# Kernel optimization log

Measured on AMD Instinct MI355X. Metric: run time of the kernel, lower is better.

## Reference

```python
import jax, jax.numpy as jnp
import numpy as np

H, C = 5, 12            # heads, head_size
N_NODES, N_EDGES = 100000, 1600000
F_NODE, F_EDGE = 128, 32
HID, N_CLASSES = 16, 2


def _lin_init(key, din, dout, bias=True):
    k1, k2 = jax.random.split(key)
    s = 1.0 / np.sqrt(din)
    W = jax.random.uniform(k1, (din, dout), minval=-s, maxval=s, dtype=jnp.float32)
    if bias:
        b = jax.random.uniform(k2, (dout,), minval=-s, maxval=s, dtype=jnp.float32)
        return W, b
    return W


def setup_inputs() -> dict:
    key = jax.random.key(0)
    ks = jax.random.split(key, 8)
    d = {}
    d["x"] = jax.random.normal(ks[0], (N_NODES, F_NODE), dtype=jnp.float32)
    d["edge_index"] = jax.random.randint(ks[1], (2, N_EDGES), 0, N_NODES)
    d["edge_attr"] = jax.random.normal(ks[2], (N_EDGES, F_EDGE), dtype=jnp.float32)
    HC = H * C
    for i, din in [(1, F_NODE), (2, HC)]:
        kk = jax.random.split(ks[2 + i], 5)
        d[f"Wq{i}"], d[f"bq{i}"] = _lin_init(kk[0], din, HC)
        d[f"Wk{i}"], d[f"bk{i}"] = _lin_init(kk[1], din, HC)
        d[f"Wv{i}"], d[f"bv{i}"] = _lin_init(kk[2], din, HC)
        d[f"We{i}"] = _lin_init(kk[3], F_EDGE, HC, bias=False)  # lin_edge has no bias in PyG
        d[f"Ws{i}"], d[f"bs{i}"] = _lin_init(kk[4], din, HC)    # root/skip linear
    d["W1"], d["b1"] = _lin_init(ks[6], HC, HID)
    d["W2"], d["b2"] = _lin_init(ks[7], HID, N_CLASSES)
    return d


def _transformer_conv(x, src, dst, edge_attr, Wq, bq, Wk, bk, Wv, bv, We, Ws, bs):
    # PyG TransformerConv, concat=True, root_weight=True, beta=False, dropout=0
    N = x.shape[0]
    q = (x @ Wq + bq).reshape(N, H, C)
    k = (x @ Wk + bk).reshape(N, H, C)
    v = (x @ Wv + bv).reshape(N, H, C)
    e = (edge_attr @ We).reshape(-1, H, C)          # [E,H,C]
    kj = k[src] + e                                  # per-edge key
    vj = v[src] + e                                  # per-edge value
    alpha = jnp.einsum('ehc,ehc->eh', q[dst], kj) / jnp.sqrt(jnp.asarray(C, x.dtype))
    # segment-softmax over incoming edges of each destination node
    amax = jax.ops.segment_max(alpha, dst, num_segments=N)          # [N,H]
    w = jnp.exp(alpha - amax[dst])
    denom = jax.ops.segment_sum(w, dst, num_segments=N)             # [N,H]
    w = w / (denom[dst] + 1e-16)
    out = jax.ops.segment_sum(vj * w[:, :, None], dst, num_segments=N).reshape(N, H * C)
    return out + x @ Ws + bs                                         # skip/root connection


def reference(x, edge_index, edge_attr,
              Wq1, bq1, Wk1, bk1, Wv1, bv1, We1, Ws1, bs1,
              Wq2, bq2, Wk2, bk2, Wv2, bv2, We2, Ws2, bs2,
              W1, b1, W2, b2):
    src, dst = edge_index[0], edge_index[1]
    h = jax.nn.relu(_transformer_conv(x, src, dst, edge_attr, Wq1, bq1, Wk1, bk1, Wv1, bv1, We1, Ws1, bs1))
    h = jax.nn.relu(_transformer_conv(h, src, dst, edge_attr, Wq2, bq2, Wk2, bk2, Wv2, bv2, We2, Ws2, bs2))
    h = jax.nn.relu(h @ W1 + b1)
    return h @ W2 + b2
```

## Files before the change

kernel.cpp:

```cpp
#include <hip/hip_runtime.h>
#include <hip/hip_bf16.h>
#include <cstddef>

#define NN 100000
#define NE 1600000
#define NH 5
#define NC 12
#define HC 60
#define FN 128
#define FE 32
#define HID 16
#define NCLS 2

template<int DIN>
__global__ __launch_bounds__(256) void qkvs_kernel(
    const float* __restrict__ X,
    const float* __restrict__ Wq, const float* __restrict__ bq,
    const float* __restrict__ Wk, const float* __restrict__ bk,
    const float* __restrict__ Wv, const float* __restrict__ bv,
    const float* __restrict__ Ws, const float* __restrict__ bs,
    float* __restrict__ q, float* __restrict__ k,
    float* __restrict__ v, float* __restrict__ s)
{
    constexpr int NB = 8;
    __shared__ float xs[NB][DIN];
    const int n0 = blockIdx.x * NB;
    for (int i = threadIdx.x; i < NB * DIN; i += 256) {
        const int m = i / DIN, r = i - m * DIN;
        const int node = n0 + m;
        xs[m][r] = (node < NN) ? X[(size_t)node * DIN + r] : 0.f;
    }
    __syncthreads();

    const int j = threadIdx.x;
    if (j >= 240) return;
    const int mat = j / 60, col = j - mat * 60;
    const float* W; const float* b; float* out;
    switch (mat) {
        case 0:  W = Wq; b = bq; out = q; break;
        case 1:  W = Wk; b = bk; out = k; break;
        case 2:  W = Wv; b = bv; out = v; break;
        default: W = Ws; b = bs; out = s; break;
    }
    float acc[NB];
    #pragma unroll
    for (int m = 0; m < NB; ++m) acc[m] = 0.f;
    #pragma unroll 4
    for (int r = 0; r < DIN; ++r) {
        const float w = W[r * 60 + col];
        #pragma unroll
        for (int m = 0; m < NB; ++m) acc[m] = fmaf(xs[m][r], w, acc[m]);
    }
    const float bb = b[col];
    #pragma unroll
    for (int m = 0; m < NB; ++m) {
        const int node = n0 + m;
        if (node < NN) out[(size_t)node * 60 + col] = acc[m] + bb;
    }
}

__global__ __launch_bounds__(256) void hist_kernel(
    const int* __restrict__ ei, int* __restrict__ cnt)
{
    const int e = blockIdx.x * 256 + threadIdx.x;
    if (e < NE) atomicAdd(&cnt[ei[NE + e]], 1);
}

__global__ __launch_bounds__(1024) void scan1_kernel(
    const int* __restrict__ cnt, int* __restrict__ excl, int* __restrict__ bsum)
{
    __shared__ int sh[1024];
    const int i = blockIdx.x * 1024 + threadIdx.x;
    const int v = (i < NN) ? cnt[i] : 0;
    sh[threadIdx.x] = v;
    __syncthreads();
    for (int off = 1; off < 1024; off <<= 1) {
        const int t = (threadIdx.x >= off) ? sh[threadIdx.x - off] : 0;
        __syncthreads();
        sh[threadIdx.x] += t;
        __syncthreads();
    }
    if (i < NN) excl[i] = sh[threadIdx.x] - v;
    if (threadIdx.x == 1023) bsum[blockIdx.x] = sh[1023];
}

__global__ void scan2_kernel(int* __restrict__ bsum, int nb, int* __restrict__ start)
{
    if (threadIdx.x == 0 && blockIdx.x == 0) {
        int acc = 0;
        for (int b = 0; b < nb; ++b) { const int t = bsum[b]; bsum[b] = acc; acc += t; }
        start[NN] = acc;
    }
}

__global__ __launch_bounds__(1024) void scan3_kernel(
    int* __restrict__ start, const int* __restrict__ bsum)
{
    const int i = blockIdx.x * 1024 + threadIdx.x;
    if (i < NN) start[i] += bsum[blockIdx.x];
}

__global__ __launch_bounds__(256) void scatter_kernel(
    const int* __restrict__ ei, int* __restrict__ cursor,
    int* __restrict__ perm, int* __restrict__ srcs)
{
    const int e = blockIdx.x * 256 + threadIdx.x;
    if (e >= NE) return;
    const int d = ei[NE + e];
    const int pos = atomicAdd(&cursor[d], 1);
    perm[pos] = e;
    srcs[pos] = ei[e];
}

__global__ __launch_bounds__(256) void agg_kernel(
    const int* __restrict__ perm, const int* __restrict__ srcs,
    const int* __restrict__ start,
    const float* __restrict__ ea, const float* __restrict__ We,
    const float* __restrict__ q, const float* __restrict__ k,
    const float* __restrict__ v, const float* __restrict__ sk,
    float* __restrict__ hout)
{
    const int wv    = threadIdx.x >> 6;
    const int lane  = threadIdx.x & 63;
    const int n     = blockIdx.x * 4 + wv;
    const int hc    = (lane < 60) ? lane : 0;
    const int hd    = hc / NC;
    const int hbase = hd * NC;
    const int c     = hc - hbase;

    const int r1 = hbase + ((c + 6) % 12);
    const int r2 = hbase + ((c + 3) % 12);
    const int r3 = hbase + ((c + 1) % 3);
    const int r4 = hbase + ((c + 2) % 3);

    float Wcol[FE];
    #pragma unroll
    for (int r = 0; r < FE; ++r) Wcol[r] = We[r * 60 + hc];

    const float qv = q[(size_t)n * 60 + hc];
    const float sv = sk[(size_t)n * 60 + hc];

    const int s0 = __builtin_amdgcn_readfirstlane(start[n]);
    const int s1 = __builtin_amdgcn_readfirstlane(start[n + 1]);

    float acc = 0.f, den = 0.f;

    for (int c0 = s0; c0 < s1; c0 += 64) {
        const int cnt = min(64, s1 - c0);

        int myE = 0, myS = 0;
        if (c0 + lane < s1) { myE = perm[c0 + lane]; myS = srcs[c0 + lane]; }

        float eaA[FE], eaB[FE], kvA, vvA, kvB, vvB;

        {
            const int e = __builtin_amdgcn_readfirstlane(__shfl(myE, 0));
            const int s = __builtin_amdgcn_readfirstlane(__shfl(myS, 0));
            const float* __restrict__ er = ea + (size_t)e * FE;
            #pragma unroll
            for (int r = 0; r < FE; ++r) eaA[r] = er[r];
            kvA = k[(size_t)s * 60 + hc];
            vvA = v[(size_t)s * 60 + hc];
        }

        for (int t = 0; t < cnt; t += 2) {
            if (t + 1 < cnt) {
                const int e = __builtin_amdgcn_readfirstlane(__shfl(myE, t + 1));
                const int s = __builtin_amdgcn_readfirstlane(__shfl(myS, t + 1));
                const float* __restrict__ er = ea + (size_t)e * FE;
                #pragma unroll
                for (int r = 0; r < FE; ++r) eaB[r] = er[r];
                kvB = k[(size_t)s * 60 + hc];
                vvB = v[(size_t)s * 60 + hc];
            }
            {
                float e0 = 0.f, e1 = 0.f;
                #pragma unroll
                for (int r = 0; r < FE; r += 2) {
                    e0 = fmaf(eaA[r],     Wcol[r],     e0);
                    e1 = fmaf(eaA[r + 1], Wcol[r + 1], e1);
                }
                const float eacc = e0 + e1;
                const float p  = qv * (kvA + eacc);
                const float f1 = p  + __shfl(p,  r1);
                const float f2 = f1 + __shfl(f1, r2);
                const float a  = f2 + __shfl(f2, r3) + __shfl(f2, r4);
                const float w  = __expf(fmaf(a, 0.28867513459481287f, -20.0f));
                acc = fmaf(w, vvA + eacc, acc);
                den += w;
            }
            if (t + 2 < cnt) {
                const int e = __builtin_amdgcn_readfirstlane(__shfl(myE, t + 2));
                const int s = __builtin_amdgcn_readfirstlane(__shfl(myS, t + 2));
                const float* __restrict__ er = ea + (size_t)e * FE;
                #pragma unroll
                for (int r = 0; r < FE; ++r) eaA[r] = er[r];
                kvA = k[(size_t)s * 60 + hc];
                vvA = v[(size_t)s * 60 + hc];
            }
            if (t + 1 < cnt) {
                float e0 = 0.f, e1 = 0.f;
                #pragma unroll
                for (int r = 0; r < FE; r += 2) {
                    e0 = fmaf(eaB[r],     Wcol[r],     e0);
                    e1 = fmaf(eaB[r + 1], Wcol[r + 1], e1);
                }
                const float eacc = e0 + e1;
                const float p  = qv * (kvB + eacc);
                const float f1 = p  + __shfl(p,  r1);
                const float f2 = f1 + __shfl(f1, r2);
                const float a  = f2 + __shfl(f2, r3) + __shfl(f2, r4);
                const float w  = __expf(fmaf(a, 0.28867513459481287f, -20.0f));
                acc = fmaf(w, vvB + eacc, acc);
                den += w;
            }
        }
    }

    if (lane < 60)
        hout[(size_t)n * 60 + hc] = fmaxf(acc / (den + 1e-16f) + sv, 0.f);
}

__global__ __launch_bounds__(256) void mlp_kernel(
    const float* __restrict__ h,
    const float* __restrict__ W1, const float* __restrict__ b1,
    const float* __restrict__ W2, const float* __restrict__ b2,
    float* __restrict__ out)
{
    __shared__ float sW1[60 * HID];
    __shared__ float sb1[HID];
    __shared__ float sW2[HID * NCLS];
    __shared__ float sb2[NCLS];
    for (int i = threadIdx.x; i < 60 * HID; i += 256) sW1[i] = W1[i];
    if (threadIdx.x < HID)        sb1[threadIdx.x] = b1[threadIdx.x];
    if (threadIdx.x < HID * NCLS) sW2[threadIdx.x] = W2[threadIdx.x];
    if (threadIdx.x < NCLS)       sb2[threadIdx.x] = b2[threadIdx.x];
    __syncthreads();

    const int n = blockIdx.x * 256 + threadIdx.x;
    if (n >= NN) return;
    const float* __restrict__ hr = h + (size_t)n * 60;
    float hv[60];
    #pragma unroll
    for (int i = 0; i < 15; ++i) {
        const float4 t = ((const float4*)hr)[i];
        hv[4 * i + 0] = t.x; hv[4 * i + 1] = t.y;
        hv[4 * i + 2] = t.z; hv[4 * i + 3] = t.w;
    }
    float o0 = sb2[0], o1 = sb2[1];
    for (int j = 0; j < HID; ++j) {
        float t = sb1[j];
        #pragma unroll
        for (int i = 0; i < 60; ++i) t = fmaf(hv[i], sW1[i * HID + j], t);
        t = fmaxf(t, 0.f);
        o0 = fmaf(t, sW2[2 * j + 0], o0);
        o1 = fmaf(t, sW2[2 * j + 1], o1);
    }
    out[(size_t)n * 2 + 0] = o0;
    out[(size_t)n * 2 + 1] = o1;
}

extern "C" void kernel_launch(void* const* d_in, const int* in_sizes, int n_in,
                              void* d_out, int out_size, void* d_ws, size_t ws_size,
                              hipStream_t stream)
{
    const float* x   = (const float*)d_in[0];
    const int*   ei  = (const int*)  d_in[1];
    const float* ea  = (const float*)d_in[2];
    const float* Wq1 = (const float*)d_in[3];  const float* bq1 = (const float*)d_in[4];
    const float* Wk1 = (const float*)d_in[5];  const float* bk1 = (const float*)d_in[6];
    const float* Wv1 = (const float*)d_in[7];  const float* bv1 = (const float*)d_in[8];
    const float* We1 = (const float*)d_in[9];
    const float* Ws1 = (const float*)d_in[10]; const float* bs1 = (const float*)d_in[11];
    const float* Wq2 = (const float*)d_in[12]; const float* bq2 = (const float*)d_in[13];
    const float* Wk2 = (const float*)d_in[14]; const float* bk2 = (const float*)d_in[15];
    const float* Wv2 = (const float*)d_in[16]; const float* bv2 = (const float*)d_in[17];
    const float* We2 = (const float*)d_in[18];
    const float* Ws2 = (const float*)d_in[19]; const float* bs2 = (const float*)d_in[20];
    const float* W1  = (const float*)d_in[21]; const float* b1  = (const float*)d_in[22];
    const float* W2  = (const float*)d_in[23]; const float* b2  = (const float*)d_in[24];
    float* out = (float*)d_out;

    float* ws = (float*)d_ws;
    const size_t NHC = (size_t)NN * 60;
    float* qb = ws;
    float* kb = qb + NHC;
    float* vb = kb + NHC;
    float* sb = vb + NHC;
    float* h0 = sb + NHC;
    int* cnt    = (int*)(h0 + NHC);
    int* startp = cnt + NN;
    int* cursor = startp + NN + 1;
    int* bsum   = cursor + NN;
    int* perm   = bsum + 128;
    int* srcs   = perm + NE;

    const int qkvs_blocks = (NN + 7) / 8;
    const int e256_blocks = NE / 256;
    const int scan_blocks = (NN + 1023) / 1024;
    const int agg_blocks  = NN / 4;
    const int mlp_blocks  = (NN + 255) / 256;

    hipMemsetAsync(cnt, 0, (size_t)NN * sizeof(int), stream);
    hist_kernel<<<e256_blocks, 256, 0, stream>>>(ei, cnt);
    scan1_kernel<<<scan_blocks, 1024, 0, stream>>>(cnt, startp, bsum);
    scan2_kernel<<<1, 64, 0, stream>>>(bsum, scan_blocks, startp);
    scan3_kernel<<<scan_blocks, 1024, 0, stream>>>(startp, bsum);
    hipMemcpyAsync(cursor, startp, (size_t)NN * sizeof(int),
                   hipMemcpyDeviceToDevice, stream);
    scatter_kernel<<<e256_blocks, 256, 0, stream>>>(ei, cursor, perm, srcs);

    qkvs_kernel<FN><<<qkvs_blocks, 256, 0, stream>>>(
        x, Wq1, bq1, Wk1, bk1, Wv1, bv1, Ws1, bs1, qb, kb, vb, sb);
    agg_kernel<<<agg_blocks, 256, 0, stream>>>(
        perm, srcs, startp, ea, We1, qb, kb, vb, sb, h0);

    qkvs_kernel<HC><<<qkvs_blocks, 256, 0, stream>>>(
        h0, Wq2, bq2, Wk2, bk2, Wv2, bv2, Ws2, bs2, qb, kb, vb, sb);
    agg_kernel<<<agg_blocks, 256, 0, stream>>>(
        perm, srcs, startp, ea, We2, qb, kb, vb, sb, h0);

    mlp_kernel<<<mlp_blocks, 256, 0, stream>>>(h0, W1, b1, W2, b2, out);
}
```

Baseline: 1.398 ms.

## Pre-permute edge attributes into CSR order and deepen k/v prefetch in aggregation

Adds a kernel that gathers edge_attr rows into destination-sorted order once, so both aggregation passes read edge features contiguously instead of through the perm indirection. The aggregation loop now prefetches source k/v two edges ahead and uses readlane in place of shfl+readfirstlane. The qkvs kernel drops its shared-memory staging of X and reads rows directly from global memory, and it also drops the node-bounds checks, which holds only because NN is divisible by 8. The permuted copy costs an extra 205MB write and read and depends on the workspace being large enough, falling back to the old path otherwise.

```diff
diff --git a/kernel.cpp b/kernel.cpp
--- a/kernel.cpp
+++ b/kernel.cpp
@@ -1,5 +1,4 @@
 #include <hip/hip_runtime.h>
-#include <hip/hip_bf16.h>
 #include <cstddef>
 
 #define NN 100000
@@ -23,15 +22,7 @@
     float* __restrict__ v, float* __restrict__ s)
 {
     constexpr int NB = 8;
-    __shared__ float xs[NB][DIN];
     const int n0 = blockIdx.x * NB;
-    for (int i = threadIdx.x; i < NB * DIN; i += 256) {
-        const int m = i / DIN, r = i - m * DIN;
-        const int node = n0 + m;
-        xs[m][r] = (node < NN) ? X[(size_t)node * DIN + r] : 0.f;
-    }
-    __syncthreads();
-
     const int j = threadIdx.x;
     if (j >= 240) return;
     const int mat = j / 60, col = j - mat * 60;
@@ -42,6 +33,7 @@
         case 2:  W = Wv; b = bv; out = v; break;
         default: W = Ws; b = bs; out = s; break;
     }
+    const float* __restrict__ xr = X + (size_t)n0 * DIN;
     float acc[NB];
     #pragma unroll
     for (int m = 0; m < NB; ++m) acc[m] = 0.f;
@@ -49,14 +41,13 @@
     for (int r = 0; r < DIN; ++r) {
         const float w = W[r * 60 + col];
         #pragma unroll
-        for (int m = 0; m < NB; ++m) acc[m] = fmaf(xs[m][r], w, acc[m]);
+        for (int m = 0; m < NB; ++m)
+            acc[m] = fmaf(xr[(size_t)m * DIN + r], w, acc[m]);
     }
     const float bb = b[col];
     #pragma unroll
-    for (int m = 0; m < NB; ++m) {
-        const int node = n0 + m;
-        if (node < NN) out[(size_t)node * 60 + col] = acc[m] + bb;
-    }
+    for (int m = 0; m < NB; ++m)
+        out[(size_t)(n0 + m) * 60 + col] = acc[m] + bb;
 }
 
 __global__ __launch_bounds__(256) void hist_kernel(
@@ -112,6 +103,18 @@
     srcs[pos] = ei[e];
 }
 
+__global__ __launch_bounds__(256) void permea_kernel(
+    const int* __restrict__ perm, const float* __restrict__ ea,
+    float* __restrict__ eaP)
+{
+    const int t = blockIdx.x * 256 + threadIdx.x;
+    const int slot = t >> 3, r4 = t & 7;
+    const int e = perm[slot];
+    const float4 val = ((const float4*)(ea + (size_t)e * FE))[r4];
+    ((float4*)(eaP + (size_t)slot * FE))[r4] = val;
+}
+
+template<bool LIN>
 __global__ __launch_bounds__(256) void agg_kernel(
     const int* __restrict__ perm, const int* __restrict__ srcs,
     const int* __restrict__ start,
@@ -145,75 +148,80 @@
 
     float acc = 0.f, den = 0.f;
 
+    auto compute = [&](const float (&EA)[FE], float KV, float VV) {
+        float e0 = 0.f, e1 = 0.f;
+        #pragma unroll
+        for (int r = 0; r < FE; r += 2) {
+            e0 = fmaf(EA[r],     Wcol[r],     e0);
+            e1 = fmaf(EA[r + 1], Wcol[r + 1], e1);
+        }
+        const float eacc = e0 + e1;
+        const float p  = qv * (KV + eacc);
+        const float f1 = p  + __shfl(p,  r1);
+        const float f2 = f1 + __shfl(f1, r2);
+        const float a  = f2 + __shfl(f2, r3) + __shfl(f2, r4);
+        const float w  = __expf(fmaf(a, 0.28867513459481287f, -20.0f));
+        acc = fmaf(w, VV + eacc, acc);
+        den += w;
+    };
+
     for (int c0 = s0; c0 < s1; c0 += 64) {
         const int cnt = min(64, s1 - c0);
 
         int myE = 0, myS = 0;
-        if (c0 + lane < s1) { myE = perm[c0 + lane]; myS = srcs[c0 + lane]; }
-
-        float eaA[FE], eaB[FE], kvA, vvA, kvB, vvB;
+        if (c0 + lane < s1) {
+            myS = srcs[c0 + lane];
+            if (!LIN) myE = perm[c0 + lane];
+        }
+
+        float eaA[FE], eaB[FE];
+        float kA = 0.f, vA = 0.f, kB = 0.f, vB = 0.f;
+        float kC = 0.f, vC = 0.f, kD = 0.f, vD = 0.f;
 
         {
-            const int e = __builtin_amdgcn_readfirstlane(__shfl(myE, 0));
-            const int s = __builtin_amdgcn_readfirstlane(__shfl(myS, 0));
-            const float* __restrict__ er = ea + (size_t)e * FE;
+            const int sA = __builtin_amdgcn_readlane(myS, 0);
+            kA = k[(size_t)sA * 60 + hc];
+            vA = v[(size_t)sA * 60 + hc];
+            if (cnt > 1) {
+                const int sB = __builtin_amdgcn_readlane(myS, 1);
+                kB = k[(size_t)sB * 60 + hc];
+                vB = v[(size_t)sB * 60 + hc];
+            }
+            const float* __restrict__ er = LIN
+                ? (ea + (size_t)c0 * FE)
+                : (ea + (size_t)__builtin_amdgcn_readlane(myE, 0) * FE);
             #pragma unroll
             for (int r = 0; r < FE; ++r) eaA[r] = er[r];
-            kvA = k[(size_t)s * 60 + hc];
-            vvA = v[(size_t)s * 60 + hc];
         }
 
         for (int t = 0; t < cnt; t += 2) {
             if (t + 1 < cnt) {
-                const int e = __builtin_amdgcn_readfirstlane(__shfl(myE, t + 1));
-                const int s = __builtin_amdgcn_readfirstlane(__shfl(myS, t + 1));
-                const float* __restrict__ er = ea + (size_t)e * FE;
+                const float* __restrict__ er = LIN
+                    ? (ea + (size_t)(c0 + t + 1) * FE)
+                    : (ea + (size_t)__builtin_amdgcn_readlane(myE, t + 1) * FE);
                 #pragma unroll
                 for (int r = 0; r < FE; ++r) eaB[r] = er[r];
-                kvB = k[(size_t)s * 60 + hc];
-                vvB = v[(size_t)s * 60 + hc];
-            }
-            {
-                float e0 = 0.f, e1 = 0.f;
-                #pragma unroll
-                for (int r = 0; r < FE; r += 2) {
-                    e0 = fmaf(eaA[r],     Wcol[r],     e0);
-                    e1 = fmaf(eaA[r + 1], Wcol[r + 1], e1);
-                }
-                const float eacc = e0 + e1;
-                const float p  = qv * (kvA + eacc);
-                const float f1 = p  + __shfl(p,  r1);
-                const float f2 = f1 + __shfl(f1, r2);
-                const float a  = f2 + __shfl(f2, r3) + __shfl(f2, r4);
-                const float w  = __expf(fmaf(a, 0.28867513459481287f, -20.0f));
-                acc = fmaf(w, vvA + eacc, acc);
-                den += w;
             }
             if (t + 2 < cnt) {
-                const int e = __builtin_amdgcn_readfirstlane(__shfl(myE, t + 2));
-                const int s = __builtin_amdgcn_readfirstlane(__shfl(myS, t + 2));
-                const float* __restrict__ er = ea + (size_t)e * FE;
+                const int sC = __builtin_amdgcn_readlane(myS, t + 2);
+                kC = k[(size_t)sC * 60 + hc];
+                vC = v[(size_t)sC * 60 + hc];
+            }
+            compute(eaA, kA, vA);
+            if (t + 2 < cnt) {
+                const float* __restrict__ er = LIN
+                    ? (ea + (size_t)(c0 + t + 2) * FE)
+                    : (ea + (size_t)__builtin_amdgcn_readlane(myE, t + 2) * FE);
                 #pragma unroll
                 for (int r = 0; r < FE; ++r) eaA[r] = er[r];
-                kvA = k[(size_t)s * 60 + hc];
-                vvA = v[(size_t)s * 60 + hc];
-            }
-            if (t + 1 < cnt) {
-                float e0 = 0.f, e1 = 0.f;
-                #pragma unroll
-                for (int r = 0; r < FE; r += 2) {
-                    e0 = fmaf(eaB[r],     Wcol[r],     e0);
-                    e1 = fmaf(eaB[r + 1], Wcol[r + 1], e1);
-                }
-                const float eacc = e0 + e1;
-                const float p  = qv * (kvB + eacc);
-                const float f1 = p  + __shfl(p,  r1);
-                const float f2 = f1 + __shfl(f1, r2);
-                const float a  = f2 + __shfl(f2, r3) + __shfl(f2, r4);
-                const float w  = __expf(fmaf(a, 0.28867513459481287f, -20.0f));
-                acc = fmaf(w, vvB + eacc, acc);
-                den += w;
-            }
+            }
+            if (t + 3 < cnt) {
+                const int sD = __builtin_amdgcn_readlane(myS, t + 3);
+                kD = k[(size_t)sD * 60 + hc];
+                vD = v[(size_t)sD * 60 + hc];
+            }
+            if (t + 1 < cnt) compute(eaB, kB, vB);
+            kA = kC; vA = vC; kB = kD; vB = vD;
         }
     }
 
@@ -281,25 +289,30 @@
     const float* W2  = (const float*)d_in[23]; const float* b2  = (const float*)d_in[24];
     float* out = (float*)d_out;
 
-    float* ws = (float*)d_ws;
-    const size_t NHC = (size_t)NN * 60;
-    float* qb = ws;
-    float* kb = qb + NHC;
-    float* vb = kb + NHC;
-    float* sb = vb + NHC;
-    float* h0 = sb + NHC;
-    int* cnt    = (int*)(h0 + NHC);
+    int* cnt    = (int*)d_ws;
     int* startp = cnt + NN;
     int* cursor = startp + NN + 1;
     int* bsum   = cursor + NN;
     int* perm   = bsum + 128;
     int* srcs   = perm + NE;
-
-    const int qkvs_blocks = (NN + 7) / 8;
+    const size_t int_bytes = (size_t)(3 * NN + 1 + 128 + 2 * NE) * sizeof(int);
+    const size_t f_off = (int_bytes + 255) & ~(size_t)255;
+    const size_t NHC = (size_t)NN * 60;
+    float* qb = (float*)((char*)d_ws + f_off);
+    float* kb = qb + NHC;
+    float* vb = kb + NHC;
+    float* sb = vb + NHC;
+    float* h0 = sb + NHC;
+    float* eaP = h0 + NHC;
+    const size_t need = f_off + 5 * NHC * sizeof(float) + (size_t)NE * FE * sizeof(float);
+    const bool lin = ws_size >= need;
+
+    const int qkvs_blocks = NN / 8;
     const int e256_blocks = NE / 256;
     const int scan_blocks = (NN + 1023) / 1024;
     const int agg_blocks  = NN / 4;
     const int mlp_blocks  = (NN + 255) / 256;
+    const int perm_blocks = NE * 8 / 256;
 
     hipMemsetAsync(cnt, 0, (size_t)NN * sizeof(int), stream);
     hist_kernel<<<e256_blocks, 256, 0, stream>>>(ei, cnt);
@@ -309,16 +322,26 @@
     hipMemcpyAsync(cursor, startp, (size_t)NN * sizeof(int),
                    hipMemcpyDeviceToDevice, stream);
     scatter_kernel<<<e256_blocks, 256, 0, stream>>>(ei, cursor, perm, srcs);
+    if (lin)
+        permea_kernel<<<perm_blocks, 256, 0, stream>>>(perm, ea, eaP);
 
     qkvs_kernel<FN><<<qkvs_blocks, 256, 0, stream>>>(
         x, Wq1, bq1, Wk1, bk1, Wv1, bv1, Ws1, bs1, qb, kb, vb, sb);
-    agg_kernel<<<agg_blocks, 256, 0, stream>>>(
-        perm, srcs, startp, ea, We1, qb, kb, vb, sb, h0);
+    if (lin)
+        agg_kernel<true><<<agg_blocks, 256, 0, stream>>>(
+            perm, srcs, startp, eaP, We1, qb, kb, vb, sb, h0);
+    else
+        agg_kernel<false><<<agg_blocks, 256, 0, stream>>>(
+            perm, srcs, startp, ea, We1, qb, kb, vb, sb, h0);
 
     qkvs_kernel<HC><<<qkvs_blocks, 256, 0, stream>>>(
         h0, Wq2, bq2, Wk2, bk2, Wv2, bv2, Ws2, bs2, qb, kb, vb, sb);
-    agg_kernel<<<agg_blocks, 256, 0, stream>>>(
-        perm, srcs, startp, ea, We2, qb, kb, vb, sb, h0);
+    if (lin)
+        agg_kernel<true><<<agg_blocks, 256, 0, stream>>>(
+            perm, srcs, startp, eaP, We2, qb, kb, vb, sb, h0);
+    else
+        agg_kernel<false><<<agg_blocks, 256, 0, stream>>>(
+            perm, srcs, startp, ea, We2, qb, kb, vb, sb, h0);
 
     mlp_kernel<<<mlp_blocks, 256, 0, stream>>>(h0, W1, b1, W2, b2, out);
 }
```

After: 1.264 ms. 9.6% less time.
